# Kernel tuning notes

Hardware: AMD Instinct MI355X
Metric: run time of the kernel (lower is better)

## Reference

```python
import jax, jax.numpy as jnp
import numpy as np

# dimensions
N = 50000    # nodes
E = 600000   # edges
NS = 64      # scalar (0e) channels of node features
NV = 32      # vector (1o) channels of node features
A = 16       # node attr channels (16x0e)
R = 8        # edge embedding dim (radial basis, 8x0e)
H = 8        # fc_hidden_size
AVG_NB = 12.0  # avg_num_neighbors
# gate layout: NS scalars (silu) + NV gate scalars (sigmoid) gating NV vectors
GS = NS + NV  # 96 scalar channels before gate
NW = NS + NS + NV + NV  # 192 per-edge TP weights (paths: s*Y0->0e, s*Y1->1o, v*Y0->1o, v.Y1->0e)


def setup_inputs() -> dict:
    key = jax.random.key(0)
    ks = jax.random.split(key, 20)
    d = {
        'node_s': jax.random.normal(ks[0], (N, NS), jnp.float32),
        'node_v': jax.random.normal(ks[1], (N, NV, 3), jnp.float32),
        'node_attrs': jax.random.normal(ks[2], (N, A), jnp.float32),
        'edge_emb': jax.random.uniform(ks[3], (E, R), jnp.float32),
        'edge_sh0': jnp.ones((E, 1), jnp.float32),
        'edge_sh1': jax.random.normal(ks[4], (E, 3), jnp.float32),
        'edge_index': jax.random.randint(ks[5], (2, E), 0, N),
        # linear_1 on node feats (per-irrep channel mixing)
        'W1s': jax.random.normal(ks[6], (NS, NS), jnp.float32),
        'W1v': jax.random.normal(ks[7], (NV, NV), jnp.float32),
        # radial MLP producing per-edge TP weights
        'Wm1': jax.random.normal(ks[8], (R, H), jnp.float32),
        'Wm2': jax.random.normal(ks[9], (H, NW), jnp.float32),
        # linear_2: TP out (96x0e+96x1o) -> pre-gate (96x0e+32x1o)
        'W2s': jax.random.normal(ks[10], (GS, GS), jnp.float32),
        'W2v': jax.random.normal(ks[11], (NS + NV, NV), jnp.float32),
        # update UVU TP internal weights (msg x attrs)
        'Wt0': jax.random.normal(ks[12], (NS, A), jnp.float32),
        'Wt1': jax.random.normal(ks[13], (NV, A), jnp.float32),
        # linear_3
        'W3s': jax.random.normal(ks[14], (NS, GS), jnp.float32),
        'W3v': jax.random.normal(ks[15], (NV, NV), jnp.float32),
        # self connection: FullyConnectedTensorProduct(node_feats, attrs -> pre-gate)
        'Wsc0': jax.random.normal(ks[16], (NS, A, GS), jnp.float32),
        'Wsc1': jax.random.normal(ks[17], (NV, A, NV), jnp.float32),
    }
    return d


def _gate(s_all, v):
    # s_all: [.., GS]; first NS scalars -> silu, last NV -> sigmoid gates for vectors
    scal = jax.nn.silu(s_all[..., :NS])
    gates = jax.nn.sigmoid(s_all[..., NS:])
    return scal, v * gates[..., None]


def reference(node_s, node_v, node_attrs, edge_emb, edge_sh0, edge_sh1, edge_index,
              W1s, W1v, Wm1, Wm2, W2s, W2v, Wt0, Wt1, W3s, W3v, Wsc0, Wsc1):
    src, dst = edge_index[0], edge_index[1]

    # ---- message ----
    s1 = (node_s @ W1s) / jnp.sqrt(jnp.float32(NS))                       # [N,NS]
    v1 = jnp.einsum('nuc,uv->nvc', node_v, W1v) / jnp.sqrt(jnp.float32(NV))
    ss = s1[src]   # [E,NS]
    vv = v1[src]   # [E,NV,3]

    # per-edge TP weights from radial MLP
    w = jax.nn.silu(edge_emb @ Wm1) @ Wm2                                 # [E,NW]
    w0a, w1a, w1b, w0b = jnp.split(w, [NS, 2 * NS, 2 * NS + NV], axis=1)

    # UVU tensor product with SH edge attrs (lmax=1)
    t0a = w0a * ss * edge_sh0                                             # [E,NS] 0e
    t0b = w0b * jnp.einsum('euc,ec->eu', vv, edge_sh1)                    # [E,NV] 0e
    t1a = w1a[:, :, None] * ss[:, :, None] * edge_sh1[:, None, :]         # [E,NS,3] 1o
    t1b = w1b[:, :, None] * vv * edge_sh0[:, :, None]                     # [E,NV,3] 1o
    tp_s = jnp.concatenate([t0a, t0b], axis=1)                            # [E,96]
    tp_v = jnp.concatenate([t1a, t1b], axis=1)                            # [E,96,3]

    m_s = (tp_s @ W2s) / jnp.sqrt(jnp.float32(GS))                        # [E,GS]
    m_v = jnp.einsum('euc,uv->evc', tp_v, W2v) / jnp.sqrt(jnp.float32(NS + NV))  # [E,NV,3]
    msg_s, msg_v = _gate(m_s, m_v)                                        # [E,NS], [E,NV,3]

    # ---- update ----
    agg_s = jax.ops.segment_sum(msg_s, dst, num_segments=N) / jnp.sqrt(jnp.float32(AVG_NB))
    agg_v = jax.ops.segment_sum(msg_v, dst, num_segments=N) / jnp.sqrt(jnp.float32(AVG_NB))

    u0 = jnp.einsum('nu,na,ua->nu', agg_s, node_attrs, Wt0) / jnp.sqrt(jnp.float32(A))
    u1 = jnp.einsum('nuc,na,ua->nuc', agg_v, node_attrs, Wt1) / jnp.sqrt(jnp.float32(A))

    f_s = (u0 @ W3s) / jnp.sqrt(jnp.float32(NS))                          # [N,GS]
    f_v = jnp.einsum('nuc,uv->nvc', u1, W3v) / jnp.sqrt(jnp.float32(NV))  # [N,NV,3]

    # self connection (fully connected TP with scalar attrs)
    sc_s = jnp.einsum('nu,na,uav->nv', node_s, node_attrs, Wsc0) / jnp.sqrt(jnp.float32(NS * A))
    sc_v = jnp.einsum('nuc,na,uaw->nwc', node_v, node_attrs, Wsc1) / jnp.sqrt(jnp.float32(NV * A))
    f_s = f_s + sc_s
    f_v = f_v + sc_v

    out_s, out_v = _gate(f_s, f_v)                                        # [N,NS], [N,NV,3]
    return jnp.concatenate([out_s, out_v.reshape(N, NV * 3)], axis=1)     # [N,160]
```

## Files before the change

### kernel.cpp

```cpp
#include <hip/hip_runtime.h>
#include <math.h>

#define N 50000
#define E 600000
#define EPB 16
#define LDK 104

typedef __attribute__((ext_vector_type(8))) short short8;
typedef __attribute__((ext_vector_type(4))) float float4v;

__device__ __forceinline__ float silu_f(float x) { return x / (1.f + __expf(-x)); }
__device__ __forceinline__ float sigm_f(float x) { return 1.f / (1.f + __expf(-x)); }
__device__ __forceinline__ unsigned short f2bf(float f) {
  unsigned u = __float_as_uint(f);
  u += 0x7fff + ((u >> 16) & 1);
  return (unsigned short)(u >> 16);
}
__device__ __forceinline__ float bf2f(unsigned short u) {
  return __uint_as_float(((unsigned)u) << 16);
}

__global__ void k_hist(const int* __restrict__ eidx, int* __restrict__ counts) {
  int e = blockIdx.x * 256 + threadIdx.x;
  if (e < E) atomicAdd(&counts[eidx[E + e]], 1);
}

__global__ __launch_bounds__(1024)
void k_scan(const int* __restrict__ counts, int* __restrict__ row_ptr) {
  __shared__ int ssum[1024];
  const int t = threadIdx.x;
  const int CH = 49;
  int lo = t * CH, hi = min(lo + CH, N);
  int s = 0;
  for (int i = lo; i < hi; i++) s += counts[i];
  ssum[t] = s;
  __syncthreads();
  for (int off = 1; off < 1024; off <<= 1) {
    int v = (t >= off) ? ssum[t - off] : 0;
    __syncthreads();
    ssum[t] += v;
    __syncthreads();
  }
  int run = (t == 0) ? 0 : ssum[t - 1];
  for (int i = lo; i < hi; i++) { row_ptr[i] = run; run += counts[i]; }
  if (t == 1023) row_ptr[N] = ssum[1023];
}

__global__ void k_scatter(const int* __restrict__ eidx, const int* __restrict__ row_ptr,
                          int* __restrict__ woff, int* __restrict__ perm) {
  int e = blockIdx.x * 256 + threadIdx.x;
  if (e < E) {
    int d = eidx[E + e];
    int p = atomicAdd(&woff[d], 1);
    perm[row_ptr[d] + p] = e;
  }
}

__global__ void k_prep(const float* __restrict__ Wsc0, const float* __restrict__ W3s,
                       const float* __restrict__ Wsc1, const float* __restrict__ W3v,
                       const float* __restrict__ W2s, const float* __restrict__ W2v,
                       unsigned short* __restrict__ BT, unsigned short* __restrict__ B2T,
                       unsigned short* __restrict__ w2sTg, unsigned short* __restrict__ w2vTg) {
  const float isq96 = 0.10206207261596575f;
  int i = blockIdx.x * 256 + threadIdx.x;
  if (i < 96 * 1088) {
    int j = i / 1088, k = i % 1088;
    float v;
    if (k < 1024) v = Wsc0[(size_t)k * 96 + j] * 0.03125f;
    else          v = W3s[(size_t)(k - 1024) * 96 + j] * 0.125f;
    BT[i] = f2bf(v);
  } else if (i < 96 * 1088 + 32 * 576) {
    int i2 = i - 96 * 1088;
    int w = i2 / 576, k = i2 % 576;
    float v = 0.f;
    if (k < 512)      v = Wsc1[(size_t)k * 32 + w] * 0.04419417382415922f;
    else if (k < 544) v = W3v[(size_t)(k - 512) * 32 + w] * 0.17677669529663689f;
    B2T[i2] = f2bf(v);
  } else if (i < 96 * 1088 + 32 * 576 + 96 * 96) {
    int i3 = i - (96 * 1088 + 32 * 576);
    int j = i3 / 96, k = i3 % 96;
    w2sTg[i3] = f2bf(W2s[(size_t)k * 96 + j] * isq96);
  } else {
    int i4 = i - (96 * 1088 + 32 * 576 + 96 * 96);
    if (i4 < 32 * 96) {
      int v = i4 / 96, u = i4 % 96;
      w2vTg[i4] = f2bf(W2v[(size_t)u * 32 + v] * isq96);
    }
  }
}

__global__ __launch_bounds__(256, 4)
void k_lin1(const float* __restrict__ node_s, const float* __restrict__ node_v,
            const float* __restrict__ W1s, const float* __restrict__ W1v,
            float* __restrict__ s1, float* __restrict__ v1) {
  __shared__ float w1s[64 * 64];
  __shared__ float w1v[32 * 32];
  for (int i = threadIdx.x; i < 64 * 64; i += 256) w1s[i] = W1s[i];
  for (int i = threadIdx.x; i < 32 * 32; i += 256) w1v[i] = W1v[i];
  __syncthreads();
  const float is_ns = 0.125f;
  const float is_nv = 0.17677669529663689f;
  int gtid = blockIdx.x * 256 + threadIdx.x;
  int stride = gridDim.x * 256;
  for (int i = gtid; i < N * 160; i += stride) {
    int n = i / 160, ch = i % 160;
    if (ch < 64) {
      const float* row = node_s + n * 64;
      float acc = 0.f;
#pragma unroll
      for (int u = 0; u < 64; u++) acc += row[u] * w1s[u * 64 + ch];
      s1[n * 64 + ch] = acc * is_ns;
    } else {
      int p = ch - 64, v = p / 3, c = p % 3;
      const float* row = node_v + n * 96;
      float acc = 0.f;
#pragma unroll
      for (int u = 0; u < 32; u++) acc += row[u * 3 + c] * w1v[u * 32 + v];
      v1[n * 96 + p] = acc * is_nv;
    }
  }
}

template<int STORE>
__global__ __launch_bounds__(256, 4)
void k_msg(const float* __restrict__ s1, const float* __restrict__ v1,
           const float* __restrict__ emb, const float* __restrict__ sh0g,
           const float* __restrict__ sh1g, const int* __restrict__ eidx,
           const int* __restrict__ perm,
           const float* __restrict__ Wm1, const float* __restrict__ Wm2,
           const unsigned short* __restrict__ w2sTg, const unsigned short* __restrict__ w2vTg,
           float* __restrict__ aggs, float* __restrict__ aggv) {
  __shared__ float wm2s[192 * 9];
  __shared__ float wm1s[64];
  __shared__ unsigned short tps[EPB * LDK];
  __shared__ unsigned short tpv[EPB * 3 * LDK];
  __shared__ float gat[EPB][33];
  __shared__ float msL[EPB][65];
  __shared__ float mvL[EPB][97];
  __shared__ float hb[EPB][8];
  __shared__ float sh1b[EPB][4];
  __shared__ float sh0b[EPB];
  __shared__ int ssrc[EPB];
  __shared__ int sdst[EPB];

  const int t = threadIdx.x;
  const int wave = t >> 6, lane = t & 63;
  const int lm = lane & 15, quad = lane >> 4;
  const int subc = t & 15;

  for (int i = t; i < 192 * 8; i += 256) {
    int h = i / 192, c = i % 192;
    wm2s[c * 9 + h] = Wm2[i];
  }
  if (t < 64) wm1s[t] = Wm1[t];

  short8 b1fr[2][3], b2fr[3];
  {
    const int nt0 = wave;
    const int nt1 = (wave + 4 < 6) ? wave + 4 : wave;
    const int nv2 = wave & 1;
#pragma unroll
    for (int kk = 0; kk < 3; kk++) {
      b1fr[0][kk] = *(const short8*)&w2sTg[(nt0 * 16 + lm) * 96 + kk * 32 + quad * 8];
      b1fr[1][kk] = *(const short8*)&w2sTg[(nt1 * 16 + lm) * 96 + kk * 32 + quad * 8];
      b2fr[kk]    = *(const short8*)&w2vTg[(nv2 * 16 + lm) * 96 + kk * 32 + quad * 8];
    }
  }
  __syncthreads();

  for (int pass = blockIdx.x; pass < E / EPB; pass += gridDim.x) {
    const int ebase = pass * EPB;
    __syncthreads();
    if (t < EPB) {
      const int e = STORE ? perm[ebase + t] : (ebase + t);
      ssrc[t] = eidx[e];
      sdst[t] = eidx[E + e];
      sh0b[t] = sh0g[e];
    } else if (t >= 64 && t < 64 + EPB * 3) {
      int i = t - 64;
      const int el = i / 3, c = i % 3;
      const int e = STORE ? perm[ebase + el] : (ebase + el);
      sh1b[el][c] = sh1g[e * 3 + c];
    } else if (t >= 128) {
      int i = t - 128, el = i >> 3, sub = i & 7;
      const int e = STORE ? perm[ebase + el] : (ebase + el);
      float acc = 0.f;
#pragma unroll
      for (int r = 0; r < 8; r++) acc += emb[e * 8 + r] * wm1s[r * 8 + sub];
      hb[el][sub] = silu_f(acc);
    }
    __syncthreads();
    {
      const int el = t >> 4, sub = subc;
      const int src = ssrc[el];
      const float s0v = sh0b[el];
      const float x0 = sh1b[el][0], x1 = sh1b[el][1], x2 = sh1b[el][2];
      float hr[8];
#pragma unroll
      for (int h = 0; h < 8; h++) hr[h] = hb[el][h];
      const float4v ss = *(const float4v*)&s1[(size_t)src * 64 + sub * 4];
      unsigned short tsv[4], tvv[3][4];
#pragma unroll
      for (int i = 0; i < 4; i++) {
        float w0a = 0.f, w1a = 0.f;
#pragma unroll
        for (int h = 0; h < 8; h++) {
          w0a += hr[h] * wm2s[(sub * 4 + i) * 9 + h];
          w1a += hr[h] * wm2s[(64 + sub * 4 + i) * 9 + h];
        }
        const float ssu = ss[i];
        tsv[i] = f2bf(w0a * ssu * s0v);
        const float base = w1a * ssu;
        tvv[0][i] = f2bf(base * x0);
        tvv[1][i] = f2bf(base * x1);
        tvv[2][i] = f2bf(base * x2);
      }
      *(uint2*)&tps[el * LDK + sub * 4] = *(uint2*)tsv;
#pragma unroll
      for (int c = 0; c < 3; c++)
        *(uint2*)&tpv[(el * 3 + c) * LDK + sub * 4] = *(uint2*)tvv[c];
      const float2* vp = (const float2*)&v1[(size_t)src * 96 + sub * 6];
      const float2 va = vp[0], vb = vp[1], vc = vp[2];
      const float v6[6] = {va.x, va.y, vb.x, vb.y, vc.x, vc.y};
      unsigned short ts2[2], tv2[3][2];
#pragma unroll
      for (int i2 = 0; i2 < 2; i2++) {
        float w1b = 0.f, w0b = 0.f;
#pragma unroll
        for (int h = 0; h < 8; h++) {
          w1b += hr[h] * wm2s[(128 + sub * 2 + i2) * 9 + h];
          w0b += hr[h] * wm2s[(160 + sub * 2 + i2) * 9 + h];
        }
        const float vx = v6[i2 * 3 + 0], vy = v6[i2 * 3 + 1], vz = v6[i2 * 3 + 2];
        ts2[i2] = f2bf(w0b * (vx * x0 + vy * x1 + vz * x2));
        tv2[0][i2] = f2bf(w1b * vx * s0v);
        tv2[1][i2] = f2bf(w1b * vy * s0v);
        tv2[2][i2] = f2bf(w1b * vz * s0v);
      }
      *(unsigned*)&tps[el * LDK + 64 + sub * 2] = *(unsigned*)ts2;
#pragma unroll
      for (int c = 0; c < 3; c++)
        *(unsigned*)&tpv[(el * 3 + c) * LDK + 64 + sub * 2] = *(unsigned*)tv2[c];
    }
    __syncthreads();
    {
      short8 afr[3];
#pragma unroll
      for (int kk = 0; kk < 3; kk++)
        afr[kk] = *(const short8*)&tps[lm * LDK + kk * 32 + quad * 8];
#pragma unroll
      for (int t2 = 0; t2 < 2; t2++) {
        const int nt = wave + t2 * 4;
        if (nt < 6) {
          float4v acc = {0.f, 0.f, 0.f, 0.f};
#pragma unroll
          for (int kk = 0; kk < 3; kk++)
            acc = __builtin_amdgcn_mfma_f32_16x16x32_bf16(afr[kk], b1fr[t2][kk], acc, 0, 0, 0);
          const int j = nt * 16 + lm;
#pragma unroll
          for (int reg = 0; reg < 4; reg++) {
            const int e = quad * 4 + reg;
            const float val = acc[reg];
            if (j < 64) {
              if (STORE) msL[e][j] = silu_f(val);
              else atomicAdd(&aggs[(size_t)sdst[e] * 64 + j], silu_f(val));
            } else {
              gat[e][j - 64] = sigm_f(val);
            }
          }
        }
      }
    }
    __syncthreads();
#pragma unroll
    for (int t2 = 0; t2 < 2; t2++) {
      const int tile = wave + t2 * 4;
      if (tile < 6) {
        const int mt = tile >> 1, nt2 = tile & 1;
        float4v acc = {0.f, 0.f, 0.f, 0.f};
#pragma unroll
        for (int kk = 0; kk < 3; kk++) {
          short8 a = *(const short8*)&tpv[(mt * 16 + lm) * LDK + kk * 32 + quad * 8];
          acc = __builtin_amdgcn_mfma_f32_16x16x32_bf16(a, b2fr[kk], acc, 0, 0, 0);
        }
        const int v = nt2 * 16 + lm;
#pragma unroll
        for (int reg = 0; reg < 4; reg++) {
          const int r = mt * 16 + quad * 4 + reg;
          const int e = (r * 171) >> 9, c = r - 3 * e;
          const float val = acc[reg] * gat[e][v];
          if (STORE) mvL[e][v * 3 + c] = val;
          else atomicAdd(&aggv[(size_t)sdst[e] * 96 + v * 3 + c], val);
        }
      }
    }
    if (STORE) {
      __syncthreads();
      if (t < 160) {
        float acc = 0.f;
        int cur = sdst[0];
        for (int s2 = 0; s2 < EPB; s2++) {
          const int d = sdst[s2];
          const float val = (t < 64) ? msL[s2][t] : mvL[s2][t - 64];
          if (d != cur) {
            if (t < 64) atomicAdd(&aggs[(size_t)cur * 64 + t], acc);
            else        atomicAdd(&aggv[(size_t)cur * 96 + (t - 64)], acc);
            acc = 0.f; cur = d;
          }
          acc += val;
        }
        if (t < 64) atomicAdd(&aggs[(size_t)cur * 64 + t], acc);
        else        atomicAdd(&aggv[(size_t)cur * 96 + (t - 64)], acc);
      }
    }
  }
}

__global__ __launch_bounds__(256, 4)
void k_c1(const float* __restrict__ node_s, const float* __restrict__ attrs,
          const float* __restrict__ aggs, const float* __restrict__ Wt0,
          const unsigned short* __restrict__ BT,
          float* __restrict__ out, float* __restrict__ gates) {
  __shared__ float s_row[32][64];
  __shared__ float attr[32][16];
  __shared__ float t0[32][64];
  __shared__ float wt0[1024];
  __shared__ unsigned short As[32 * 72];
  const int t = threadIdx.x;
  const int wave = t >> 6, lane = t & 63, lm = lane & 15, quad = lane >> 4;
  const int nbase = blockIdx.x * 32;

  for (int i = t; i < 1024; i += 256) wt0[i] = Wt0[i];
  for (int i = t; i < 2048; i += 256) {
    int nl = i >> 6, u = i & 63, n = nbase + nl;
    s_row[nl][u] = (n < N) ? node_s[(size_t)n * 64 + u] : 0.f;
    t0[nl][u]    = (n < N) ? aggs[(size_t)n * 64 + u] : 0.f;
  }
  for (int i = t; i < 512; i += 256) {
    int nl = i >> 4, a = i & 15, n = nbase + nl;
    attr[nl][a] = (n < N) ? attrs[(size_t)n * 16 + a] : 0.f;
  }
  __syncthreads();
  for (int i = t; i < 2048; i += 256) {
    int nl = i >> 6, u = i & 63;
    float d0 = 0.f;
#pragma unroll
    for (int a = 0; a < 16; a++) d0 += attr[nl][a] * wt0[u * 16 + a];
    t0[nl][u] *= d0 * 0.07216878364870322f;
  }

  float4v acc[3] = {{0,0,0,0},{0,0,0,0},{0,0,0,0}};
  int mts[3], nts[3];
#pragma unroll
  for (int tt = 0; tt < 3; tt++) {
    const int tile = wave + tt * 4;
    mts[tt] = tile / 6;
    nts[tt] = tile % 6;
  }

  for (int kc = 0; kc < 17; kc++) {
    __syncthreads();
    {
      const int row = t >> 3, c0 = (t & 7) * 8;
      unsigned short tmp[8];
      if (kc < 16) {
        const int u = kc * 4 + (c0 >> 4);
        const float sval = s_row[row][u];
        const int ab = c0 & 8;
#pragma unroll
        for (int i = 0; i < 8; i++) tmp[i] = f2bf(sval * attr[row][ab + i]);
      } else {
#pragma unroll
        for (int i = 0; i < 8; i++) tmp[i] = f2bf(t0[row][c0 + i]);
      }
      *(uint4*)&As[row * 72 + c0] = *(uint4*)tmp;
    }
    __syncthreads();
#pragma unroll
    for (int ks = 0; ks < 2; ks++) {
      short8 am0 = *(const short8*)&As[(lm) * 72 + ks * 32 + quad * 8];
      short8 am1 = *(const short8*)&As[(16 + lm) * 72 + ks * 32 + quad * 8];
#pragma unroll
      for (int tt = 0; tt < 3; tt++) {
        short8 b = *(const short8*)&BT[(size_t)(nts[tt] * 16 + lm) * 1088 + kc * 64 + ks * 32 + quad * 8];
        acc[tt] = __builtin_amdgcn_mfma_f32_16x16x32_bf16(mts[tt] ? am1 : am0, b, acc[tt], 0, 0, 0);
      }
    }
  }
#pragma unroll
  for (int tt = 0; tt < 3; tt++) {
    const int j = nts[tt] * 16 + lm;
#pragma unroll
    for (int reg = 0; reg < 4; reg++) {
      const int m = mts[tt] * 16 + quad * 4 + reg;
      const int n = nbase + m;
      if (n < N) {
        const float val = acc[tt][reg];
        if (j < 64) out[(size_t)n * 160 + j] = silu_f(val);
        else        gates[(size_t)n * 32 + (j - 64)] = sigm_f(val);
      }
    }
  }
}

__global__ __launch_bounds__(256, 3)
void k_c2(const float* __restrict__ node_v, const float* __restrict__ attrs,
          const float* __restrict__ aggv, const float* __restrict__ Wt1,
          const unsigned short* __restrict__ B2T, const float* __restrict__ gts,
          float* __restrict__ out) {
  __shared__ float nvs[32][96];
  __shared__ float t1s[32][96];
  __shared__ float attr[32][16];
  __shared__ float wt1[512];
  __shared__ unsigned short As2[96 * 72];
  const int t = threadIdx.x;
  const int wave = t >> 6, lane = t & 63, lm = lane & 15, quad = lane >> 4;
  const int nbase = blockIdx.x * 32;

  for (int i = t; i < 512; i += 256) wt1[i] = Wt1[i];
  for (int i = t; i < 32 * 96; i += 256) {
    int nl = i / 96, rr = i % 96, n = nbase + nl;
    nvs[nl][rr] = (n < N) ? node_v[(size_t)n * 96 + rr] : 0.f;
    t1s[nl][rr] = (n < N) ? aggv[(size_t)n * 96 + rr] : 0.f;
  }
  for (int i = t; i < 512; i += 256) {
    int nl = i >> 4, a = i & 15, n = nbase + nl;
    attr[nl][a] = (n < N) ? attrs[(size_t)n * 16 + a] : 0.f;
  }
  __syncthreads();
  for (int i = t; i < 1024; i += 256) {
    int nl = i >> 5, u = i & 31;
    float d1 = 0.f;
#pragma unroll
    for (int a = 0; a < 16; a++) d1 += attr[nl][a] * wt1[u * 16 + a];
    d1 *= 0.07216878364870322f;
    t1s[nl][u * 3 + 0] *= d1; t1s[nl][u * 3 + 1] *= d1; t1s[nl][u * 3 + 2] *= d1;
  }

  float4v acc[3] = {{0,0,0,0},{0,0,0,0},{0,0,0,0}};
  int mts[3], nts[3];
#pragma unroll
  for (int tt = 0; tt < 3; tt++) {
    const int tile = wave + tt * 4;
    mts[tt] = tile >> 1;
    nts[tt] = tile & 1;
  }

  for (int kc = 0; kc < 9; kc++) {
    __syncthreads();
#pragma unroll
    for (int jj = 0; jj < 3; jj++) {
      const int job = t + jj * 256;
      const int row = job >> 3, c0 = (job & 7) * 8;
      const int nl = (row * 171) >> 9, c = row - 3 * nl;
      const int kbase = kc * 64 + c0;
      unsigned short tmp[8];
      if (kbase < 512) {
        const int u = kbase >> 4;
        const float vval = nvs[nl][u * 3 + c];
        const int ab = c0 & 8;
#pragma unroll
        for (int i = 0; i < 8; i++) tmp[i] = f2bf(vval * attr[nl][ab + i]);
      } else if (kbase < 544) {
        const int u2 = kbase - 512;
#pragma unroll
        for (int i = 0; i < 8; i++) tmp[i] = f2bf(t1s[nl][(u2 + i) * 3 + c]);
      } else {
#pragma unroll
        for (int i = 0; i < 8; i++) tmp[i] = 0;
      }
      *(uint4*)&As2[row * 72 + c0] = *(uint4*)tmp;
    }
    __syncthreads();
#pragma unroll
    for (int ks = 0; ks < 2; ks++) {
#pragma unroll
      for (int tt = 0; tt < 3; tt++) {
        short8 a = *(const short8*)&As2[(mts[tt] * 16 + lm) * 72 + ks * 32 + quad * 8];
        short8 b = *(const short8*)&B2T[(size_t)(nts[tt] * 16 + lm) * 576 + kc * 64 + ks * 32 + quad * 8];
        acc[tt] = __builtin_amdgcn_mfma_f32_16x16x32_bf16(a, b, acc[tt], 0, 0, 0);
      }
    }
  }
#pragma unroll
  for (int tt = 0; tt < 3; tt++) {
    const int w = nts[tt] * 16 + lm;
#pragma unroll
    for (int reg = 0; reg < 4; reg++) {
      const int row = mts[tt] * 16 + quad * 4 + reg;
      const int nl = (row * 171) >> 9, c = row - 3 * nl;
      const int n = nbase + nl;
      if (n < N)
        out[(size_t)n * 160 + 64 + w * 3 + c] = acc[tt][reg] * gts[(size_t)n * 32 + w];
    }
  }
}

extern "C" void kernel_launch(void* const* d_in, const int* in_sizes, int n_in,
                              void* d_out, int out_size, void* d_ws, size_t ws_size,
                              hipStream_t stream) {
  const float* node_s = (const float*)d_in[0];
  const float* node_v = (const float*)d_in[1];
  const float* attrs  = (const float*)d_in[2];
  const float* emb    = (const float*)d_in[3];
  const float* sh0    = (const float*)d_in[4];
  const float* sh1    = (const float*)d_in[5];
  const int*   eidx   = (const int*)d_in[6];
  const float* W1s    = (const float*)d_in[7];
  const float* W1v    = (const float*)d_in[8];
  const float* Wm1    = (const float*)d_in[9];
  const float* Wm2    = (const float*)d_in[10];
  const float* W2s    = (const float*)d_in[11];
  const float* W2v    = (const float*)d_in[12];
  const float* Wt0    = (const float*)d_in[13];
  const float* Wt1    = (const float*)d_in[14];
  const float* W3s    = (const float*)d_in[15];
  const float* W3v    = (const float*)d_in[16];
  const float* Wsc0   = (const float*)d_in[17];
  const float* Wsc1   = (const float*)d_in[18];

  char* p = (char*)d_ws;
  float* s1  = (float*)p;  p += (size_t)N * 64 * 4;
  float* v1f = (float*)p;  p += (size_t)N * 96 * 4;
  float* gts = (float*)p;  p += (size_t)N * 32 * 4;
  unsigned short* BT    = (unsigned short*)p;  p += (size_t)96 * 1088 * 2;
  unsigned short* B2T   = (unsigned short*)p;  p += (size_t)32 * 576 * 2;
  unsigned short* w2sTg = (unsigned short*)p;  p += (size_t)96 * 96 * 2;
  unsigned short* w2vTg = (unsigned short*)p;  p += (size_t)32 * 96 * 2;
  char* pmode = p;
  size_t base = (size_t)(pmode - (char*)d_ws);
  size_t need_store = base + ((size_t)N + 1) * 4 + (size_t)N * 4 + (size_t)N * 4
                    + (size_t)E * 4 + (size_t)N * 160 * 4;
  const bool store = (ws_size >= need_store);

  k_prep<<<528, 256, 0, stream>>>(Wsc0, W3s, Wsc1, W3v, W2s, W2v, BT, B2T, w2sTg, w2vTg);
  k_lin1<<<1024, 256, 0, stream>>>(node_s, node_v, W1s, W1v, s1, v1f);

  if (store) {
    int* rowp = (int*)pmode;
    int* cnt  = rowp + (N + 1);
    int* woff = cnt + N;
    int* perm = woff + N;
    float* aggs = (float*)(perm + E);
    float* aggv = aggs + (size_t)N * 64;
    hipMemsetAsync(cnt, 0, (size_t)N * 2 * 4, stream);
    hipMemsetAsync(aggs, 0, (size_t)N * 160 * 4, stream);
    k_hist<<<(E + 255) / 256, 256, 0, stream>>>(eidx, cnt);
    k_scan<<<1, 1024, 0, stream>>>(cnt, rowp);
    k_scatter<<<(E + 255) / 256, 256, 0, stream>>>(eidx, rowp, woff, perm);
    k_msg<1><<<1024, 256, 0, stream>>>(s1, v1f, emb, sh0, sh1, eidx, perm, Wm1, Wm2,
                                       w2sTg, w2vTg, aggs, aggv);
    k_c1<<<1563, 256, 0, stream>>>(node_s, attrs, aggs, Wt0, BT, (float*)d_out, gts);
    k_c2<<<1563, 256, 0, stream>>>(node_v, attrs, aggv, Wt1, B2T, gts, (float*)d_out);
  } else {
    float* aggs = (float*)pmode;
    float* aggv = aggs + (size_t)N * 64;
    hipMemsetAsync(aggs, 0, (size_t)N * 160 * 4, stream);
    k_msg<0><<<1024, 256, 0, stream>>>(s1, v1f, emb, sh0, sh1, eidx, nullptr, Wm1, Wm2,
                                       w2sTg, w2vTg, aggs, aggv);
    k_c1<<<1563, 256, 0, stream>>>(node_s, attrs, aggs, Wt0, BT, (float*)d_out, gts);
    k_c2<<<1563, 256, 0, stream>>>(node_v, attrs, aggv, Wt1, B2T, gts, (float*)d_out);
  }
}
```

Baseline: 716.1 us.

## Build MFMA A-operands in registers, dropping LDS staging and per-chunk barriers

In k_c1 and k_c2, each lane now builds its MFMA A fragment directly in registers from the shared source rows and attribute values cached in registers. This replaces the cooperative write to an LDS staging tile and the two __syncthreads per K-chunk. Source arrays are padded by one column to reduce bank conflicts, k_c2 skips its all-zero final half-chunk, and k_c2's launch bound is raised to 4 blocks. The cost is redundant bf16 conversion across lanes (k_c1 converts both row halves every step), plus higher register pressure that could limit occupancy.

```diff
diff --git a/kernel.cpp b/kernel.cpp
--- a/kernel.cpp
+++ b/kernel.cpp
@@ -321,11 +321,10 @@
           const float* __restrict__ aggs, const float* __restrict__ Wt0,
           const unsigned short* __restrict__ BT,
           float* __restrict__ out, float* __restrict__ gates) {
-  __shared__ float s_row[32][64];
+  __shared__ float s_row[32][65];
   __shared__ float attr[32][16];
-  __shared__ float t0[32][64];
+  __shared__ float t0[32][65];
   __shared__ float wt0[1024];
-  __shared__ unsigned short As[32 * 72];
   const int t = threadIdx.x;
   const int wave = t >> 6, lane = t & 63, lm = lane & 15, quad = lane >> 4;
   const int nbase = blockIdx.x * 32;
@@ -348,6 +347,15 @@
     for (int a = 0; a < 16; a++) d0 += attr[nl][a] * wt0[u * 16 + a];
     t0[nl][u] *= d0 * 0.07216878364870322f;
   }
+  __syncthreads();
+
+  const int a0 = (quad & 1) * 8;
+  float aA0[8], aA1[8];
+#pragma unroll
+  for (int i = 0; i < 8; i++) {
+    aA0[i] = attr[lm][a0 + i];
+    aA1[i] = attr[16 + lm][a0 + i];
+  }
 
   float4v acc[3] = {{0,0,0,0},{0,0,0,0},{0,0,0,0}};
   int mts[3], nts[3];
@@ -359,27 +367,28 @@
   }
 
   for (int kc = 0; kc < 17; kc++) {
-    __syncthreads();
-    {
-      const int row = t >> 3, c0 = (t & 7) * 8;
-      unsigned short tmp[8];
+#pragma unroll
+    for (int ks = 0; ks < 2; ks++) {
+      unsigned short e0[8], e1[8];
       if (kc < 16) {
-        const int u = kc * 4 + (c0 >> 4);
-        const float sval = s_row[row][u];
-        const int ab = c0 & 8;
-#pragma unroll
-        for (int i = 0; i < 8; i++) tmp[i] = f2bf(sval * attr[row][ab + i]);
+        const int u = kc * 4 + ks * 2 + (quad >> 1);
+        const float s0v = s_row[lm][u];
+        const float s1v = s_row[16 + lm][u];
+#pragma unroll
+        for (int i = 0; i < 8; i++) {
+          e0[i] = f2bf(s0v * aA0[i]);
+          e1[i] = f2bf(s1v * aA1[i]);
+        }
       } else {
-#pragma unroll
-        for (int i = 0; i < 8; i++) tmp[i] = f2bf(t0[row][c0 + i]);
-      }
-      *(uint4*)&As[row * 72 + c0] = *(uint4*)tmp;
-    }
-    __syncthreads();
-#pragma unroll
-    for (int ks = 0; ks < 2; ks++) {
-      short8 am0 = *(const short8*)&As[(lm) * 72 + ks * 32 + quad * 8];
-      short8 am1 = *(const short8*)&As[(16 + lm) * 72 + ks * 32 + quad * 8];
+        const int c0 = ks * 32 + quad * 8;
+#pragma unroll
+        for (int i = 0; i < 8; i++) {
+          e0[i] = f2bf(t0[lm][c0 + i]);
+          e1[i] = f2bf(t0[16 + lm][c0 + i]);
+        }
+      }
+      const short8 am0 = *(const short8*)e0;
+      const short8 am1 = *(const short8*)e1;
 #pragma unroll
       for (int tt = 0; tt < 3; tt++) {
         short8 b = *(const short8*)&BT[(size_t)(nts[tt] * 16 + lm) * 1088 + kc * 64 + ks * 32 + quad * 8];
@@ -403,16 +412,15 @@
   }
 }
 
-__global__ __launch_bounds__(256, 3)
+__global__ __launch_bounds__(256, 4)
 void k_c2(const float* __restrict__ node_v, const float* __restrict__ attrs,
           const float* __restrict__ aggv, const float* __restrict__ Wt1,
           const unsigned short* __restrict__ B2T, const float* __restrict__ gts,
           float* __restrict__ out) {
-  __shared__ float nvs[32][96];
-  __shared__ float t1s[32][96];
+  __shared__ float nvs[32][97];
+  __shared__ float t1s[32][97];
   __shared__ float attr[32][16];
   __shared__ float wt1[512];
-  __shared__ unsigned short As2[96 * 72];
   const int t = threadIdx.x;
   const int wave = t >> 6, lane = t & 63, lm = lane & 15, quad = lane >> 4;
   const int nbase = blockIdx.x * 32;
@@ -436,47 +444,44 @@
     d1 *= 0.07216878364870322f;
     t1s[nl][u * 3 + 0] *= d1; t1s[nl][u * 3 + 1] *= d1; t1s[nl][u * 3 + 2] *= d1;
   }
-
-  float4v acc[3] = {{0,0,0,0},{0,0,0,0},{0,0,0,0}};
-  int mts[3], nts[3];
+  __syncthreads();
+
+  int nls[3], cs[3], nts[3], mts[3];
 #pragma unroll
   for (int tt = 0; tt < 3; tt++) {
     const int tile = wave + tt * 4;
     mts[tt] = tile >> 1;
     nts[tt] = tile & 1;
-  }
+    const int row = mts[tt] * 16 + lm;
+    nls[tt] = (row * 171) >> 9;
+    cs[tt]  = row - 3 * nls[tt];
+  }
+  const int a0 = (quad & 1) * 8;
+  float aA[3][8];
+#pragma unroll
+  for (int tt = 0; tt < 3; tt++)
+#pragma unroll
+    for (int i = 0; i < 8; i++) aA[tt][i] = attr[nls[tt]][a0 + i];
+
+  float4v acc[3] = {{0,0,0,0},{0,0,0,0},{0,0,0,0}};
 
   for (int kc = 0; kc < 9; kc++) {
-    __syncthreads();
-#pragma unroll
-    for (int jj = 0; jj < 3; jj++) {
-      const int job = t + jj * 256;
-      const int row = job >> 3, c0 = (job & 7) * 8;
-      const int nl = (row * 171) >> 9, c = row - 3 * nl;
-      const int kbase = kc * 64 + c0;
-      unsigned short tmp[8];
-      if (kbase < 512) {
-        const int u = kbase >> 4;
-        const float vval = nvs[nl][u * 3 + c];
-        const int ab = c0 & 8;
-#pragma unroll
-        for (int i = 0; i < 8; i++) tmp[i] = f2bf(vval * attr[nl][ab + i]);
-      } else if (kbase < 544) {
-        const int u2 = kbase - 512;
-#pragma unroll
-        for (int i = 0; i < 8; i++) tmp[i] = f2bf(t1s[nl][(u2 + i) * 3 + c]);
-      } else {
-#pragma unroll
-        for (int i = 0; i < 8; i++) tmp[i] = 0;
-      }
-      *(uint4*)&As2[row * 72 + c0] = *(uint4*)tmp;
-    }
-    __syncthreads();
 #pragma unroll
     for (int ks = 0; ks < 2; ks++) {
+      if (kc == 8 && ks == 1) continue;
 #pragma unroll
       for (int tt = 0; tt < 3; tt++) {
-        short8 a = *(const short8*)&As2[(mts[tt] * 16 + lm) * 72 + ks * 32 + quad * 8];
+        unsigned short ev[8];
+        if (kc < 8) {
+          const int u = kc * 4 + ks * 2 + (quad >> 1);
+          const float vv = nvs[nls[tt]][u * 3 + cs[tt]];
+#pragma unroll
+          for (int i = 0; i < 8; i++) ev[i] = f2bf(vv * aA[tt][i]);
+        } else {
+#pragma unroll
+          for (int i = 0; i < 8; i++) ev[i] = f2bf(t1s[nls[tt]][(quad * 8 + i) * 3 + cs[tt]]);
+        }
+        const short8 a = *(const short8*)ev;
         short8 b = *(const short8*)&B2T[(size_t)(nts[tt] * 16 + lm) * 576 + kc * 64 + ks * 32 + quad * 8];
         acc[tt] = __builtin_amdgcn_mfma_f32_16x16x32_bf16(a, b, acc[tt], 0, 0, 0);
       }
```

Result: faster. 700.8 us (-2.1%).
